# Kernel tuning notes

Measured on AMD Instinct MI355X. Metric: run time of the kernel, lower is better.

The kernel has to match this reference:

```python
import jax, jax.numpy as jnp
import numpy as np

WIDTH = [256, 512, 256]
NUM = 5       # grid intervals -> NUM+1 grid points per edge
K = 3         # spline order
BATCH = 256
GRID_RANGE = (-1.0, 1.0)


def extend_grid(grid, k):
    # grid: (size, NUM+1) -> (size, NUM+1+2k); mirrors pykan B_batch extend
    h = (grid[:, -1:] - grid[:, :1]) / (grid.shape[1] - 1)
    for _ in range(k):
        grid = jnp.concatenate([grid[:, :1] - h, grid, grid[:, -1:] + h], axis=1)
    return grid


def b_batch(x, grid, k):
    # Cox-de Boor B-spline bases. x: (size, B); grid: (size, G) extended.
    # returns (size, G-k-1, B)
    xg = x[:, None, :]
    g = grid[:, :, None]
    B = ((xg >= g[:, :-1]) & (xg < g[:, 1:])).astype(x.dtype)
    for d in range(1, k + 1):
        left = (xg - g[:, : -(d + 1)]) / (g[:, d:-1] - g[:, : -(d + 1)])
        right = (g[:, d + 1:] - xg) / (g[:, d + 1:] - g[:, 1:-d])
        B = left * B[:, :-1] + right * B[:, 1:]
    return B


def kan_layer(x, grid, coef, scale_base, scale_sp, bias, in_dim, out_dim):
    # x: (B, in_dim); edge ordering is (out, in) flattened, matching
    # torch einsum('ij,k->ikj', x, ones(out)).reshape(B, size)
    Bn = x.shape[0]
    size = out_dim * in_dim
    xe = jnp.broadcast_to(x[:, None, :], (Bn, out_dim, in_dim)).reshape(Bn, size)
    basis = b_batch(xe.T, extend_grid(grid, K), K)        # (size, NUM+K, B)
    spl = jnp.einsum('sn,snb->bs', coef, basis)            # (B, size)
    y = scale_base[None, :] * jax.nn.silu(xe) + scale_sp[None, :] * spl
    postacts = y.reshape(Bn, out_dim, in_dim)
    x_out = postacts.sum(-1) + bias                        # bias: (1, out_dim)
    # per-edge grid stats, as in KAN.forward
    gr = grid.reshape(out_dim, in_dim, -1)
    input_range = gr[:, :, -1] - gr[:, :, 0] + 1e-4
    acts_scale = jnp.mean(jnp.abs(postacts), axis=0) / input_range
    acts_std = jnp.std(postacts, axis=0, ddof=1)           # torch.std is unbiased
    return x_out, acts_scale, acts_std


def _make_params(key):
    params = {}
    for l in range(len(WIDTH) - 1):
        i, o = WIDTH[l], WIDTH[l + 1]
        size = i * o
        k1, k2, key = jax.random.split(key, 3)
        params[f'grid{l}'] = jnp.broadcast_to(
            jnp.linspace(GRID_RANGE[0], GRID_RANGE[1], NUM + 1, dtype=jnp.float32),
            (size, NUM + 1)) + jnp.zeros((size, NUM + 1), dtype=jnp.float32)
        params[f'coef{l}'] = jax.random.normal(k1, (size, NUM + K), dtype=jnp.float32) * 0.1
        params[f'scale_base{l}'] = (1.0 / np.sqrt(i)).astype(np.float32) + \
            (jax.random.normal(k2, (size,), dtype=jnp.float32) * 2.0 - 1.0) * 0.1
        params[f'scale_sp{l}'] = jnp.ones((size,), dtype=jnp.float32)
        params[f'bias{l}'] = jnp.zeros((1, o), dtype=jnp.float32)
    return params


def setup_inputs() -> dict:
    key = jax.random.key(0)
    kx, kp = jax.random.split(key)
    inp = {'x': jax.random.normal(kx, (BATCH, WIDTH[0]), dtype=jnp.float32)}
    inp.update(_make_params(kp))
    return inp


def reference(x, grid0, coef0, scale_base0, scale_sp0, bias0,
              grid1, coef1, scale_base1, scale_sp1, bias1):
    x, sc0, st0 = kan_layer(x, grid0, coef0, scale_base0, scale_sp0, bias0, WIDTH[0], WIDTH[1])
    x, sc1, st1 = kan_layer(x, grid1, coef1, scale_base1, scale_sp1, bias1, WIDTH[1], WIDTH[2])
    return x, sc0, st0, sc1, st1
```

## Files before the change

### kernel.cpp

```cpp
#include <hip/hip_runtime.h>
#include <math.h>

constexpr int BATCH = 256;

typedef short short8 __attribute__((ext_vector_type(8)));
typedef float f32x4 __attribute__((ext_vector_type(4)));
typedef float f32x16 __attribute__((ext_vector_type(16)));

__device__ __forceinline__ unsigned short f2bf(float f) {
    unsigned int u = __float_as_uint(f);
    u += 0x7FFFu + ((u >> 16) & 1u);
    return (unsigned short)(u >> 16);
}
__device__ __forceinline__ unsigned int pack2(float a, float b) {
    return (unsigned int)f2bf(a) | ((unsigned int)f2bf(b) << 16);
}

__device__ __forceinline__ void basis_eval(
    float x, const float* __restrict__ grid, int ii, float out[9])
{
    float g[6];
#pragma unroll
    for (int k = 0; k < 6; ++k) g[k] = grid[(size_t)ii * 6 + k];
    float h = (g[5] - g[0]) * 0.2f;

    float t[12];
    t[0] = g[0] - 3.f * h; t[1] = g[0] - 2.f * h; t[2] = g[0] - h;
#pragma unroll
    for (int k = 0; k < 6; ++k) t[3 + k] = g[k];
    t[9] = g[5] + h; t[10] = g[5] + 2.f * h; t[11] = g[5] + 3.f * h;

    float Bv[11];
#pragma unroll
    for (int j = 0; j < 11; ++j)
        Bv[j] = (x >= t[j] && x < t[j + 1]) ? 1.0f : 0.0f;

#pragma unroll
    for (int d = 1; d <= 3; ++d) {
#pragma unroll
        for (int j = 0; j + d < 11; ++j) {
            float left  = __fdividef(x - t[j],         t[j + d] - t[j]);
            float right = __fdividef(t[j + d + 1] - x, t[j + d + 1] - t[j + 1]);
            Bv[j] = left * Bv[j] + right * Bv[j + 1];
        }
    }

#pragma unroll
    for (int k = 0; k < 8; ++k) out[k] = Bv[k];
    out[8] = __fdividef(x, 1.0f + __expf(-x));
}

__device__ __forceinline__ void store_rec16(unsigned short* rec, const float v[9])
{
    uint4* p = (uint4*)rec;
    p[0] = make_uint4(pack2(v[0], v[1]), pack2(v[2], v[3]),
                      pack2(v[4], v[5]), pack2(v[6], v[7]));
    p[1] = make_uint4(pack2(v[8], 0.f), 0u, 0u, 0u);
}

__device__ __forceinline__ void merge_body(
    const float* __restrict__ coef, const float* __restrict__ ssp,
    const float* __restrict__ sb, unsigned short* __restrict__ wc16, int s)
{
    float sspv = ssp[s], sbv = sb[s];
    const float4* c = (const float4*)(coef + (size_t)s * 8);
    float4 c0 = c[0], c1 = c[1];
    float v[9] = { sspv * c0.x, sspv * c0.y, sspv * c0.z, sspv * c0.w,
                   sspv * c1.x, sspv * c1.y, sspv * c1.z, sspv * c1.w, sbv };
    store_rec16(wc16 + (size_t)s * 16, v);
}

__device__ __forceinline__ void gemm0_fused(
    const unsigned short* __restrict__ wc16_0, const unsigned short* __restrict__ bas16_0,
    const float* __restrict__ bias0, const float* __restrict__ grid1,
    unsigned short* __restrict__ bas16_1, int bid, float (*T)[16][17])
{
    constexpr int K2 = 256 * 16, KW = K2 / 4;
    int mt = bid >> 4, nt = bid & 15;
    int t = threadIdx.x, l = t & 63, w = t >> 6;
    int m0 = mt * 16;
    int n0 = nt * 16;

    const unsigned short* pa = wc16_0  + (size_t)(m0 + (l & 15)) * K2 + w * KW + ((l >> 4) * 8);
    const unsigned short* pb = bas16_0 + (size_t)(n0 + (l & 15)) * K2 + w * KW + ((l >> 4) * 8);

    f32x4 acc = {0.f, 0.f, 0.f, 0.f};
#pragma unroll 8
    for (int kk = 0; kk < KW / 32; ++kk) {
        short8 av = *(const short8*)pa; pa += 32;
        short8 bv = *(const short8*)pb; pb += 32;
        acc = __builtin_amdgcn_mfma_f32_16x16x32_bf16(av, bv, acc, 0, 0, 0);
    }

#pragma unroll
    for (int r = 0; r < 4; ++r)
        T[w][(l >> 4) * 4 + r][l & 15] = acc[r];
    __syncthreads();

    int ii_loc = t & 15, b_loc = t >> 4;
    float d = T[0][ii_loc][b_loc] + T[1][ii_loc][b_loc]
            + T[2][ii_loc][b_loc] + T[3][ii_loc][b_loc];
    int ii = m0 + ii_loc;
    float xv = d + bias0[ii];
    float out[9];
    basis_eval(xv, grid1, ii, out);
    store_rec16(bas16_1 + ((size_t)(n0 + b_loc) * 512 + ii) * 16, out);
    __syncthreads();
}

__device__ __forceinline__ void gemm1_fused(
    const unsigned short* __restrict__ bas16_1, const unsigned short* __restrict__ wc16_1,
    const float* __restrict__ bias1, float* __restrict__ x2, int bid, float (*T)[16][17])
{
    constexpr int K2 = 512 * 16, KW = K2 / 4;
    int mt = bid >> 4, nt = bid & 15;
    int t = threadIdx.x, l = t & 63, w = t >> 6;
    int m0 = mt * 16;
    int n0 = nt * 16;

    const unsigned short* pa = bas16_1 + (size_t)(m0 + (l & 15)) * K2 + w * KW + ((l >> 4) * 8);
    const unsigned short* pb = wc16_1  + (size_t)(n0 + (l & 15)) * K2 + w * KW + ((l >> 4) * 8);

    f32x4 acc = {0.f, 0.f, 0.f, 0.f};
#pragma unroll 8
    for (int kk = 0; kk < KW / 32; ++kk) {
        short8 av = *(const short8*)pa; pa += 32;
        short8 bv = *(const short8*)pb; pb += 32;
        acc = __builtin_amdgcn_mfma_f32_16x16x32_bf16(av, bv, acc, 0, 0, 0);
    }

#pragma unroll
    for (int r = 0; r < 4; ++r)
        T[w][(l >> 4) * 4 + r][l & 15] = acc[r];
    __syncthreads();

    int o_loc = t & 15, b_loc = t >> 4;
    float d = T[0][b_loc][o_loc] + T[1][b_loc][o_loc]
            + T[2][b_loc][o_loc] + T[3][b_loc][o_loc];
    int o = n0 + o_loc;
    x2[(size_t)(m0 + b_loc) * 256 + o] = d + bias1[o];
}

template <int I>
__device__ __forceinline__ void stats_mfma(
    const unsigned short* __restrict__ bas16, const unsigned short* __restrict__ wc16,
    const float* __restrict__ grid, float* __restrict__ sc, float* __restrict__ st,
    int id)
{
    int og = id / I, ii = id % I;
    int l = threadIdx.x & 63;
    int row = l & 31, chunk = l >> 5;

    short8 bfrag = *(const short8*)(
        wc16 + ((size_t)(og * 32 + row) * I + ii) * 16 + chunk * 8);

    float ab = 0.f, sm = 0.f, sq = 0.f;
    for (int bt = 0; bt < BATCH / 32; ++bt) {
        int b = bt * 32 + row;
        short8 av = *(const short8*)(
            bas16 + ((size_t)b * I + ii) * 16 + chunk * 8);
        f32x16 d;
#pragma unroll
        for (int r = 0; r < 16; ++r) d[r] = 0.f;
        d = __builtin_amdgcn_mfma_f32_32x32x16_bf16(av, bfrag, d, 0, 0, 0);
#pragma unroll
        for (int r = 0; r < 16; ++r) {
            float y = d[r];
            ab += fabsf(y);
            sm += y;
            sq = fmaf(y, y, sq);
        }
    }

    ab += __shfl_xor(ab, 32);
    sm += __shfl_xor(sm, 32);
    sq += __shfl_xor(sq, 32);

    if (l < 32) {
        int o = og * 32 + l;
        size_t s = (size_t)o * I + ii;
        float range = grid[s * 6 + 5] - grid[s * 6] + 1e-4f;
        sc[s] = (ab * (1.0f / BATCH)) / range;
        float var = (sq - sm * sm * (1.0f / BATCH)) * (1.0f / (BATCH - 1));
        st[s] = sqrtf(fmaxf(var, 0.0f));
    }
}

__global__ __launch_bounds__(256) void k1_prep(
    const float* __restrict__ coef0, const float* __restrict__ ssp0,
    const float* __restrict__ sb0,   unsigned short* __restrict__ wc16_0,
    const float* __restrict__ coef1, const float* __restrict__ ssp1,
    const float* __restrict__ sb1,   unsigned short* __restrict__ wc16_1,
    const float* __restrict__ x, const float* __restrict__ grid0,
    unsigned short* __restrict__ bas16_0)
{
    int bid = blockIdx.x, t = threadIdx.x;
    if (bid < 512)  { merge_body(coef0, ssp0, sb0, wc16_0, bid * 256 + t); return; }
    if (bid < 1024) { merge_body(coef1, ssp1, sb1, wc16_1, (bid - 512) * 256 + t); return; }
    int tile = bid - 1024;
    int bt = tile >> 4, it = tile & 15;
    int ii = it * 16 + (t & 15), b = bt * 16 + (t >> 4);
    float out[9];
    basis_eval(x[(size_t)b * 256 + ii], grid0, ii, out);
    store_rec16(bas16_0 + ((size_t)b * 256 + ii) * 16, out);
}

__global__ __launch_bounds__(256) void k2_sweep0(
    const unsigned short* __restrict__ wc16_0, const unsigned short* __restrict__ bas16_0,
    const float* __restrict__ bias0, const float* __restrict__ grid1,
    unsigned short* __restrict__ bas16_1,
    const float* __restrict__ grid0, float* __restrict__ sc0, float* __restrict__ st0)
{
    __shared__ float Tsh[4][16][17];
    int bid = blockIdx.x;
    if (bid < 512) {
        gemm0_fused(wc16_0, bas16_0, bias0, grid1, bas16_1, bid, Tsh);
    } else {
        int id = (bid - 512) * 4 + (threadIdx.x >> 6);
        stats_mfma<256>(bas16_0, wc16_0, grid0, sc0, st0, id);
    }
}

__global__ __launch_bounds__(256) void k3_sweep1(
    const unsigned short* __restrict__ bas16_1, const unsigned short* __restrict__ wc16_1,
    const float* __restrict__ bias1, float* __restrict__ x2,
    const float* __restrict__ grid1, float* __restrict__ sc1, float* __restrict__ st1)
{
    __shared__ float Tsh[4][16][17];
    int bid = blockIdx.x;
    if (bid < 256) {
        gemm1_fused(bas16_1, wc16_1, bias1, x2, bid, Tsh);
    } else {
        int id = (bid - 256) * 4 + (threadIdx.x >> 6);
        stats_mfma<512>(bas16_1, wc16_1, grid1, sc1, st1, id);
    }
}

extern "C" void kernel_launch(void* const* d_in, const int* in_sizes, int n_in,
                              void* d_out, int out_size, void* d_ws, size_t ws_size,
                              hipStream_t stream)
{
    const float* x     = (const float*)d_in[0];
    const float* grid0 = (const float*)d_in[1];
    const float* coef0 = (const float*)d_in[2];
    const float* sb0   = (const float*)d_in[3];
    const float* ssp0  = (const float*)d_in[4];
    const float* bias0 = (const float*)d_in[5];
    const float* grid1 = (const float*)d_in[6];
    const float* coef1 = (const float*)d_in[7];
    const float* sb1   = (const float*)d_in[8];
    const float* ssp1  = (const float*)d_in[9];
    const float* bias1 = (const float*)d_in[10];

    float* out = (float*)d_out;
    float* x2  = out;
    float* sc0 = out + 65536;
    float* st0 = out + 196608;
    float* sc1 = out + 327680;
    float* st1 = out + 458752;

    char* w = (char*)d_ws;
    unsigned short* wc16_0  = (unsigned short*)w; w += (size_t)131072 * 32;
    unsigned short* wc16_1  = (unsigned short*)w; w += (size_t)131072 * 32;
    unsigned short* bas16_0 = (unsigned short*)w; w += (size_t)65536 * 32;
    unsigned short* bas16_1 = (unsigned short*)w; w += (size_t)131072 * 32;

    k1_prep<<<1280, 256, 0, stream>>>(
        coef0, ssp0, sb0, wc16_0,
        coef1, ssp1, sb1, wc16_1,
        x, grid0, bas16_0);

    k2_sweep0<<<1536, 256, 0, stream>>>(
        wc16_0, bas16_0, bias0, grid1, bas16_1, grid0, sc0, st0);

    k3_sweep1<<<1280, 256, 0, stream>>>(
        bas16_1, wc16_1, bias1, x2, grid1, sc1, st1);
}
```

Baseline: 57.10 us.

## Use 32x32 GEMM tiles, double-output stats waves, and move layer-1 weight merge

```diff
diff --git a/kernel.cpp b/kernel.cpp
--- a/kernel.cpp
+++ b/kernel.cpp
@@ -73,72 +73,100 @@
 __device__ __forceinline__ void gemm0_fused(
     const unsigned short* __restrict__ wc16_0, const unsigned short* __restrict__ bas16_0,
     const float* __restrict__ bias0, const float* __restrict__ grid1,
-    unsigned short* __restrict__ bas16_1, int bid, float (*T)[16][17])
+    unsigned short* __restrict__ bas16_1, int bid, float (*T)[32][33])
 {
     constexpr int K2 = 256 * 16, KW = K2 / 4;
-    int mt = bid >> 4, nt = bid & 15;
+    int mt = bid >> 3, nt = bid & 7;
     int t = threadIdx.x, l = t & 63, w = t >> 6;
-    int m0 = mt * 16;
-    int n0 = nt * 16;
-
-    const unsigned short* pa = wc16_0  + (size_t)(m0 + (l & 15)) * K2 + w * KW + ((l >> 4) * 8);
-    const unsigned short* pb = bas16_0 + (size_t)(n0 + (l & 15)) * K2 + w * KW + ((l >> 4) * 8);
-
-    f32x4 acc = {0.f, 0.f, 0.f, 0.f};
-#pragma unroll 8
+    int m0 = mt * 32;
+    int n0 = nt * 32;
+
+    f32x4 acc[2][2];
+#pragma unroll
+    for (int r = 0; r < 2; ++r)
+#pragma unroll
+        for (int c = 0; c < 2; ++c) acc[r][c] = {0.f, 0.f, 0.f, 0.f};
+
+#pragma unroll 4
     for (int kk = 0; kk < KW / 32; ++kk) {
-        short8 av = *(const short8*)pa; pa += 32;
-        short8 bv = *(const short8*)pb; pb += 32;
-        acc = __builtin_amdgcn_mfma_f32_16x16x32_bf16(av, bv, acc, 0, 0, 0);
-    }
-
-#pragma unroll
-    for (int r = 0; r < 4; ++r)
-        T[w][(l >> 4) * 4 + r][l & 15] = acc[r];
+        int koff = w * KW + kk * 32 + ((l >> 4) * 8);
+        short8 a0 = *(const short8*)(wc16_0  + (size_t)(m0 +      (l & 15)) * K2 + koff);
+        short8 a1 = *(const short8*)(wc16_0  + (size_t)(m0 + 16 + (l & 15)) * K2 + koff);
+        short8 b0 = *(const short8*)(bas16_0 + (size_t)(n0 +      (l & 15)) * K2 + koff);
+        short8 b1 = *(const short8*)(bas16_0 + (size_t)(n0 + 16 + (l & 15)) * K2 + koff);
+        acc[0][0] = __builtin_amdgcn_mfma_f32_16x16x32_bf16(a0, b0, acc[0][0], 0, 0, 0);
+        acc[0][1] = __builtin_amdgcn_mfma_f32_16x16x32_bf16(a0, b1, acc[0][1], 0, 0, 0);
+        acc[1][0] = __builtin_amdgcn_mfma_f32_16x16x32_bf16(a1, b0, acc[1][0], 0, 0, 0);
+        acc[1][1] = __builtin_amdgcn_mfma_f32_16x16x32_bf16(a1, b1, acc[1][1], 0, 0, 0);
+    }
+
+#pragma unroll
+    for (int r16 = 0; r16 < 2; ++r16)
+#pragma unroll
+        for (int c16 = 0; c16 < 2; ++c16)
+#pragma unroll
+            for (int r = 0; r < 4; ++r)
+                T[w][r16 * 16 + (l >> 4) * 4 + r][c16 * 16 + (l & 15)] = acc[r16][c16][r];
     __syncthreads();
 
-    int ii_loc = t & 15, b_loc = t >> 4;
-    float d = T[0][ii_loc][b_loc] + T[1][ii_loc][b_loc]
-            + T[2][ii_loc][b_loc] + T[3][ii_loc][b_loc];
-    int ii = m0 + ii_loc;
-    float xv = d + bias0[ii];
-    float out[9];
-    basis_eval(xv, grid1, ii, out);
-    store_rec16(bas16_1 + ((size_t)(n0 + b_loc) * 512 + ii) * 16, out);
+#pragma unroll
+    for (int e = t; e < 1024; e += 256) {
+        int row = e >> 5, col = e & 31;
+        float d = T[0][row][col] + T[1][row][col] + T[2][row][col] + T[3][row][col];
+        int ii = m0 + row;
+        float xv = d + bias0[ii];
+        float out[9];
+        basis_eval(xv, grid1, ii, out);
+        store_rec16(bas16_1 + ((size_t)(n0 + col) * 512 + ii) * 16, out);
+    }
     __syncthreads();
 }
 
 __device__ __forceinline__ void gemm1_fused(
     const unsigned short* __restrict__ bas16_1, const unsigned short* __restrict__ wc16_1,
-    const float* __restrict__ bias1, float* __restrict__ x2, int bid, float (*T)[16][17])
+    const float* __restrict__ bias1, float* __restrict__ x2, int bid, float (*T)[32][33])
 {
     constexpr int K2 = 512 * 16, KW = K2 / 4;
-    int mt = bid >> 4, nt = bid & 15;
+    int mt = bid >> 3, nt = bid & 7;
     int t = threadIdx.x, l = t & 63, w = t >> 6;
-    int m0 = mt * 16;
-    int n0 = nt * 16;
-
-    const unsigned short* pa = bas16_1 + (size_t)(m0 + (l & 15)) * K2 + w * KW + ((l >> 4) * 8);
-    const unsigned short* pb = wc16_1  + (size_t)(n0 + (l & 15)) * K2 + w * KW + ((l >> 4) * 8);
-
-    f32x4 acc = {0.f, 0.f, 0.f, 0.f};
-#pragma unroll 8
+    int m0 = mt * 32;
+    int n0 = nt * 32;
+
+    f32x4 acc[2][2];
+#pragma unroll
+    for (int r = 0; r < 2; ++r)
+#pragma unroll
+        for (int c = 0; c < 2; ++c) acc[r][c] = {0.f, 0.f, 0.f, 0.f};
+
+#pragma unroll 4
     for (int kk = 0; kk < KW / 32; ++kk) {
-        short8 av = *(const short8*)pa; pa += 32;
-        short8 bv = *(const short8*)pb; pb += 32;
-        acc = __builtin_amdgcn_mfma_f32_16x16x32_bf16(av, bv, acc, 0, 0, 0);
-    }
-
-#pragma unroll
-    for (int r = 0; r < 4; ++r)
-        T[w][(l >> 4) * 4 + r][l & 15] = acc[r];
+        int koff = w * KW + kk * 32 + ((l >> 4) * 8);
+        short8 a0 = *(const short8*)(bas16_1 + (size_t)(m0 +      (l & 15)) * K2 + koff);
+        short8 a1 = *(const short8*)(bas16_1 + (size_t)(m0 + 16 + (l & 15)) * K2 + koff);
+        short8 b0 = *(const short8*)(wc16_1  + (size_t)(n0 +      (l & 15)) * K2 + koff);
+        short8 b1 = *(const short8*)(wc16_1  + (size_t)(n0 + 16 + (l & 15)) * K2 + koff);
+        acc[0][0] = __builtin_amdgcn_mfma_f32_16x16x32_bf16(a0, b0, acc[0][0], 0, 0, 0);
+        acc[0][1] = __builtin_amdgcn_mfma_f32_16x16x32_bf16(a0, b1, acc[0][1], 0, 0, 0);
+        acc[1][0] = __builtin_amdgcn_mfma_f32_16x16x32_bf16(a1, b0, acc[1][0], 0, 0, 0);
+        acc[1][1] = __builtin_amdgcn_mfma_f32_16x16x32_bf16(a1, b1, acc[1][1], 0, 0, 0);
+    }
+
+#pragma unroll
+    for (int r16 = 0; r16 < 2; ++r16)
+#pragma unroll
+        for (int c16 = 0; c16 < 2; ++c16)
+#pragma unroll
+            for (int r = 0; r < 4; ++r)
+                T[w][r16 * 16 + (l >> 4) * 4 + r][c16 * 16 + (l & 15)] = acc[r16][c16][r];
     __syncthreads();
 
-    int o_loc = t & 15, b_loc = t >> 4;
-    float d = T[0][b_loc][o_loc] + T[1][b_loc][o_loc]
-            + T[2][b_loc][o_loc] + T[3][b_loc][o_loc];
-    int o = n0 + o_loc;
-    x2[(size_t)(m0 + b_loc) * 256 + o] = d + bias1[o];
+#pragma unroll
+    for (int e = t; e < 1024; e += 256) {
+        int row = e >> 5, col = e & 31;
+        float d = T[0][row][col] + T[1][row][col] + T[2][row][col] + T[3][row][col];
+        int o = n0 + col;
+        x2[(size_t)(m0 + row) * 256 + o] = d + bias1[o];
+    }
 }
 
 template <int I>
@@ -151,53 +179,57 @@
     int l = threadIdx.x & 63;
     int row = l & 31, chunk = l >> 5;
 
-    short8 bfrag = *(const short8*)(
-        wc16 + ((size_t)(og * 32 + row) * I + ii) * 16 + chunk * 8);
-
-    float ab = 0.f, sm = 0.f, sq = 0.f;
+    short8 bf0 = *(const short8*)(
+        wc16 + ((size_t)(og * 64 + row) * I + ii) * 16 + chunk * 8);
+    short8 bf1 = *(const short8*)(
+        wc16 + ((size_t)(og * 64 + 32 + row) * I + ii) * 16 + chunk * 8);
+
+    float ab0 = 0.f, sm0 = 0.f, sq0 = 0.f;
+    float ab1 = 0.f, sm1 = 0.f, sq1 = 0.f;
     for (int bt = 0; bt < BATCH / 32; ++bt) {
-        int b = bt * 32 + row;
         short8 av = *(const short8*)(
-            bas16 + ((size_t)b * I + ii) * 16 + chunk * 8);
-        f32x16 d;
-#pragma unroll
-        for (int r = 0; r < 16; ++r) d[r] = 0.f;
-        d = __builtin_amdgcn_mfma_f32_32x32x16_bf16(av, bfrag, d, 0, 0, 0);
+            bas16 + ((size_t)(bt * 32 + row) * I + ii) * 16 + chunk * 8);
+        f32x16 d0, d1;
+#pragma unroll
+        for (int r = 0; r < 16; ++r) { d0[r] = 0.f; d1[r] = 0.f; }
+        d0 = __builtin_amdgcn_mfma_f32_32x32x16_bf16(av, bf0, d0, 0, 0, 0);
+        d1 = __builtin_amdgcn_mfma_f32_32x32x16_bf16(av, bf1, d1, 0, 0, 0);
 #pragma unroll
         for (int r = 0; r < 16; ++r) {
-            float y = d[r];
-            ab += fabsf(y);
-            sm += y;
-            sq = fmaf(y, y, sq);
+            float y0 = d0[r], y1 = d1[r];
+            ab0 += fabsf(y0); sm0 += y0; sq0 = fmaf(y0, y0, sq0);
+            ab1 += fabsf(y1); sm1 += y1; sq1 = fmaf(y1, y1, sq1);
         }
     }
 
-    ab += __shfl_xor(ab, 32);
-    sm += __shfl_xor(sm, 32);
-    sq += __shfl_xor(sq, 32);
+    ab0 += __shfl_xor(ab0, 32); sm0 += __shfl_xor(sm0, 32); sq0 += __shfl_xor(sq0, 32);
+    ab1 += __shfl_xor(ab1, 32); sm1 += __shfl_xor(sm1, 32); sq1 += __shfl_xor(sq1, 32);
 
     if (l < 32) {
-        int o = og * 32 + l;
-        size_t s = (size_t)o * I + ii;
-        float range = grid[s * 6 + 5] - grid[s * 6] + 1e-4f;
-        sc[s] = (ab * (1.0f / BATCH)) / range;
-        float var = (sq - sm * sm * (1.0f / BATCH)) * (1.0f / (BATCH - 1));
-        st[s] = sqrtf(fmaxf(var, 0.0f));
+#pragma unroll
+        for (int half = 0; half < 2; ++half) {
+            float ab = half ? ab1 : ab0;
+            float sm = half ? sm1 : sm0;
+            float sq = half ? sq1 : sq0;
+            int o = og * 64 + half * 32 + l;
+            size_t s = (size_t)o * I + ii;
+            float range = grid[s * 6 + 5] - grid[s * 6] + 1e-4f;
+            sc[s] = (ab * (1.0f / BATCH)) / range;
+            float var = (sq - sm * sm * (1.0f / BATCH)) * (1.0f / (BATCH - 1));
+            st[s] = sqrtf(fmaxf(var, 0.0f));
+        }
     }
 }
 
 __global__ __launch_bounds__(256) void k1_prep(
     const float* __restrict__ coef0, const float* __restrict__ ssp0,
     const float* __restrict__ sb0,   unsigned short* __restrict__ wc16_0,
-    const float* __restrict__ coef1, const float* __restrict__ ssp1,
-    const float* __restrict__ sb1,   unsigned short* __restrict__ wc16_1,
     const float* __restrict__ x, const float* __restrict__ grid0,
     unsigned short* __restrict__ bas16_0)
 {
     int bid = blockIdx.x, t = threadIdx.x;
-    if (bid < 512)  { merge_body(coef0, ssp0, sb0, wc16_0, bid * 256 + t); return; }
-    if (bid < 1024) { merge_body(coef1, ssp1, sb1, wc16_1, (bid - 512) * 256 + t); return; }
-    int tile = bid - 1024;
+    if (bid < 512) { merge_body(coef0, ssp0, sb0, wc16_0, bid * 256 + t); return; }
+    int tile = bid - 512;
     int bt = tile >> 4, it = tile & 15;
     int ii = it * 16 + (t & 15), b = bt * 16 + (t >> 4);
     float out[9];
@@ -209,15 +241,19 @@
     const unsigned short* __restrict__ wc16_0, const unsigned short* __restrict__ bas16_0,
     const float* __restrict__ bias0, const float* __restrict__ grid1,
     unsigned short* __restrict__ bas16_1,
-    const float* __restrict__ grid0, float* __restrict__ sc0, float* __restrict__ st0)
-{
-    __shared__ float Tsh[4][16][17];
+    const float* __restrict__ grid0, float* __restrict__ sc0, float* __restrict__ st0,
+    const float* __restrict__ coef1, const float* __restrict__ ssp1,
+    const float* __restrict__ sb1,   unsigned short* __restrict__ wc16_1)
+{
+    __shared__ float Tsh[4][32][33];
     int bid = blockIdx.x;
-    if (bid < 512) {
+    if (bid < 128) {
         gemm0_fused(wc16_0, bas16_0, bias0, grid1, bas16_1, bid, Tsh);
+    } else if (bid < 640) {
+        int id = (bid - 128) * 4 + (threadIdx.x >> 6);
+        stats_mfma<256>(bas16_0, wc16_0, grid0, sc0, st0, id);
     } else {
-        int id = (bid - 512) * 4 + (threadIdx.x >> 6);
-        stats_mfma<256>(bas16_0, wc16_0, grid0, sc0, st0, id);
+        merge_body(coef1, ssp1, sb1, wc16_1, (bid - 640) * 256 + threadIdx.x);
     }
 }
 
@@ -226,12 +262,12 @@
     const float* __restrict__ bias1, float* __restrict__ x2,
     const float* __restrict__ grid1, float* __restrict__ sc1, float* __restrict__ st1)
 {
-    __shared__ float Tsh[4][16][17];
+    __shared__ float Tsh[4][32][33];
     int bid = blockIdx.x;
-    if (bid < 256) {
+    if (bid < 64) {
         gemm1_fused(bas16_1, wc16_1, bias1, x2, bid, Tsh);
     } else {
-        int id = (bid - 256) * 4 + (threadIdx.x >> 6);
+        int id = (bid - 64) * 4 + (threadIdx.x >> 6);
         stats_mfma<512>(bas16_1, wc16_1, grid1, sc1, st1, id);
     }
 }
@@ -265,14 +301,13 @@
     unsigned short* bas16_0 = (unsigned short*)w; w += (size_t)65536 * 32;
     unsigned short* bas16_1 = (unsigned short*)w; w += (size_t)131072 * 32;
 
-    k1_prep<<<1280, 256, 0, stream>>>(
-        coef0, ssp0, sb0, wc16_0,
-        coef1, ssp1, sb1, wc16_1,
-        x, grid0, bas16_0);
-
-    k2_sweep0<<<1536, 256, 0, stream>>>(
-        wc16_0, bas16_0, bias0, grid1, bas16_1, grid0, sc0, st0);
-
-    k3_sweep1<<<1280, 256, 0, stream>>>(
+    k1_prep<<<768, 256, 0, stream>>>(
+        coef0, ssp0, sb0, wc16_0, x, grid0, bas16_0);
+
+    k2_sweep0<<<1152, 256, 0, stream>>>(
+        wc16_0, bas16_0, bias0, grid1, bas16_1,
+        grid0, sc0, st0, coef1, ssp1, sb1, wc16_1);
+
+    k3_sweep1<<<576, 256, 0, stream>>>(
         bas16_1, wc16_1, bias1, x2, grid1, sc1, st1);
 }
```

After: 76.91 us. 34.7% more time.
